# Kernel tuning notes

Hardware: AMD Instinct MI355X
Metric: run time of the kernel (lower is better)

Reference implementation:

```python
import jax, jax.numpy as jnp
import numpy as np

NEG_SLOPE = 0.01  # torch F.leaky_relu default

def setup_inputs() -> dict:
    key = jax.random.key(0)
    k1, k2, k3 = jax.random.split(key, 3)
    N, V, F_in, H = 32, 1024, 128, 64
    features = jax.random.normal(k1, (N, V, F_in), dtype=jnp.float32)
    # torch nn.Linear weights: W: [H, F_in], a: [1, 2H]
    W = jax.random.normal(k2, (H, F_in), dtype=jnp.float32) * (1.0 / np.sqrt(F_in))
    a = jax.random.normal(k3, (1, 2 * H), dtype=jnp.float32) * (1.0 / np.sqrt(2 * H))
    return {"features": features, "W": W, "a": a}

def reference(features, W, a):
    N, V, _ = features.shape
    H = W.shape[0]
    # h = features @ W^T : [N, V, H]
    h = jnp.einsum('nvf,hf->nvh', features, W)
    # The concat-linear trick decomposes: a([h_i ; h_j]) = h_i @ a_src + h_j @ a_dst
    a_src = a[0, :H]   # [H]
    a_dst = a[0, H:]   # [H]
    s_src = h @ a_src  # [N, V]  (score contribution of node i)
    s_dst = h @ a_dst  # [N, V]  (score contribution of node j)
    e = s_src[:, :, None] + s_dst[:, None, :]          # [N, V, V]
    e = jnp.where(e >= 0, e, NEG_SLOPE * e)            # leaky_relu
    attention = jax.nn.softmax(e, axis=2)              # softmax over j
    h_prime = jnp.einsum('nij,njh->nih', attention, h) # [N, V, H]
    return h_prime
```

## Files before the change

kernel.cpp:

```cpp
#include <hip/hip_runtime.h>
#include <hip/hip_bf16.h>

#define NEG_SLOPE 0.01f

constexpr int N_G  = 32;
constexpr int V_N  = 1024;
constexpr int F_IN = 128;
constexpr int H_D  = 64;
constexpr int NV   = N_G * V_N;

typedef __attribute__((ext_vector_type(8))) short bf16x8;
typedef __attribute__((ext_vector_type(4))) float f32x4;


__global__ __launch_bounds__(256) void gat_h_kernel(
    const float* __restrict__ feat,
    const float* __restrict__ W,
    const float* __restrict__ a,
    __hip_bfloat16* __restrict__ hT,
    float* __restrict__ s_src,
    float* __restrict__ s_dst)
{
    __shared__ float Fs[64][65];
    __shared__ float WsT[64][64];
    __shared__ float red[2][4][64];

    const int tid = threadIdx.x;
    const int row = tid & 63;
    const int hq  = tid >> 6;
    const int r0  = blockIdx.x * 64;

    float acc[16];
#pragma unroll
    for (int c = 0; c < 16; ++c) acc[c] = 0.f;

    for (int kh = 0; kh < 2; ++kh) {
        __syncthreads();
#pragma unroll
        for (int t = 0; t < 4; ++t) {
            int f4 = tid + t * 256;
            int rr = f4 >> 4;
            int kk = (f4 & 15) << 2;
            float4 v = *reinterpret_cast<const float4*>(
                feat + (size_t)(r0 + rr) * F_IN + kh * 64 + kk);
            Fs[rr][kk + 0] = v.x; Fs[rr][kk + 1] = v.y;
            Fs[rr][kk + 2] = v.z; Fs[rr][kk + 3] = v.w;
        }
#pragma unroll
        for (int t = 0; t < 4; ++t) {
            int f4 = tid + t * 256;
            int hh = f4 >> 4;
            int kk = (f4 & 15) << 2;
            float4 v = *reinterpret_cast<const float4*>(
                W + (size_t)hh * F_IN + kh * 64 + kk);
            WsT[kk + 0][hh] = v.x; WsT[kk + 1][hh] = v.y;
            WsT[kk + 2][hh] = v.z; WsT[kk + 3][hh] = v.w;
        }
        __syncthreads();
#pragma unroll 8
        for (int k = 0; k < 64; ++k) {
            float fv = Fs[row][k];
            const float4* wrow = reinterpret_cast<const float4*>(&WsT[k][hq * 16]);
            float wv[16];
            *reinterpret_cast<float4*>(&wv[0])  = wrow[0];
            *reinterpret_cast<float4*>(&wv[4])  = wrow[1];
            *reinterpret_cast<float4*>(&wv[8])  = wrow[2];
            *reinterpret_cast<float4*>(&wv[12]) = wrow[3];
#pragma unroll
            for (int c = 0; c < 16; ++c) acc[c] += fv * wv[c];
        }
    }

    float ps = 0.f, pd = 0.f;
#pragma unroll
    for (int c = 0; c < 16; ++c) {
        ps += acc[c] * a[hq * 16 + c];
        pd += acc[c] * a[H_D + hq * 16 + c];
    }
    red[0][hq][row] = ps;
    red[1][hq][row] = pd;

    {
        const int g   = r0 >> 10;
        const int rl  = (r0 & (V_N - 1)) + row;
        const int jt  = rl >> 6;
        const int j   = rl & 63;
        const int kk  = (j >> 5) & 1;
        const int kg  = (j >> 3) & 3;
        const int r   = j & 7;
        char* tile = (char*)(hT + (size_t)g * H_D * V_N) + (size_t)jt * 8192;
#pragma unroll
        for (int cc = 0; cc < 16; ++cc) {
            int byteoff = ((((hq * 2 + kk) * 64) + kg * 16 + cc) << 4) + (r << 1);
            *reinterpret_cast<__hip_bfloat16*>(tile + byteoff) = __float2bfloat16(acc[cc]);
        }
    }

    __syncthreads();
    if (tid < 64) {
        s_src[r0 + tid] = red[0][0][tid] + red[0][1][tid] + red[0][2][tid] + red[0][3][tid];
    } else if (tid < 128) {
        int r = tid - 64;
        s_dst[r0 + r] = red[1][0][r] + red[1][1][r] + red[1][2][r] + red[1][3][r];
    }
}

__global__ __launch_bounds__(256) void gat_attn_mfma(
    const __hip_bfloat16* __restrict__ hT,
    const float* __restrict__ s_src,
    const float* __restrict__ s_dst,
    float* __restrict__ out)
{
    __shared__ float sd[V_N];
    __shared__ float wred[4];
    __shared__ int4 hbuf[2][512];

    const int tid  = threadIdx.x;
    const int lane = tid & 63;
    const int wv   = tid >> 6;
    const int m    = lane & 15;
    const int kg   = lane >> 4;
    const int n    = blockIdx.x >> 4;
    const int i0   = (blockIdx.x & 15) * 64;
    const size_t nbase = (size_t)n * V_N;

    const char* hTg = (const char*)(hT + (size_t)n * H_D * V_N);

    float lm;
    {
        float4 v = *reinterpret_cast<const float4*>(s_dst + nbase + tid * 4);
        *reinterpret_cast<float4*>(&sd[tid * 4]) = v;
        lm = fmaxf(fmaxf(v.x, v.y), fmaxf(v.z, v.w));
    }
#pragma unroll
    for (int off = 32; off >= 1; off >>= 1)
        lm = fmaxf(lm, __shfl_xor(lm, off));
    if (lane == 0) wred[wv] = lm;

    const int row  = i0 + wv * 16 + m;
    const float ss = s_src[nbase + row];

    {
        int4 s0 = *reinterpret_cast<const int4*>(hTg + tid * 32);
        int4 s1 = *reinterpret_cast<const int4*>(hTg + tid * 32 + 16);
        hbuf[0][tid * 2]     = s0;
        hbuf[0][tid * 2 + 1] = s1;
    }
    __syncthreads();

    const float M    = fmaxf(fmaxf(wred[0], wred[1]), fmaxf(wred[2], wred[3]));
    const float t0   = ss + M;
    const float negm = -fmaxf(t0, NEG_SLOPE * t0);

    f32x4 accC[4];
    f32x4 accD = {0.f, 0.f, 0.f, 0.f};
#pragma unroll
    for (int t = 0; t < 4; ++t) accC[t] = (f32x4){0.f, 0.f, 0.f, 0.f};

    bf16x8 ones;
#pragma unroll
    for (int r = 0; r < 8; ++r) ones[r] = (short)0x3F80;

    int cur = 0;
    for (int jt = 0; jt < V_N / 64; ++jt) {
        int4 n0, n1;
        if (jt < V_N / 64 - 1) {
            const char* g = hTg + (size_t)(jt + 1) * 8192 + tid * 32;
            n0 = *reinterpret_cast<const int4*>(g);
            n1 = *reinterpret_cast<const int4*>(g + 16);
        }

        const char* bb = (const char*)&hbuf[cur][0];
#pragma unroll
        for (int kk = 0; kk < 2; ++kk) {
            float p[8];
            *reinterpret_cast<float4*>(&p[0]) =
                *reinterpret_cast<const float4*>(&sd[jt * 64 + kk * 32 + kg * 8]);
            *reinterpret_cast<float4*>(&p[4]) =
                *reinterpret_cast<const float4*>(&sd[jt * 64 + kk * 32 + kg * 8 + 4]);

            bf16x8 A;
#pragma unroll
            for (int r = 0; r < 8; ++r) {
                float tt = ss + p[r];
                float l  = fmaxf(tt, NEG_SLOPE * tt);
                float w  = __expf(l + negm);
                A[r] = (short)__builtin_bit_cast(unsigned short, __float2bfloat16(w));
            }

            accD = __builtin_amdgcn_mfma_f32_16x16x32_bf16(A, ones, accD, 0, 0, 0);
#pragma unroll
            for (int t = 0; t < 4; ++t) {
                bf16x8 B = *reinterpret_cast<const bf16x8*>(
                    bb + (t * 2 + kk) * 1024 + lane * 16);
                accC[t] = __builtin_amdgcn_mfma_f32_16x16x32_bf16(A, B, accC[t], 0, 0, 0);
            }
        }

        if (jt < V_N / 64 - 1) {
            hbuf[cur ^ 1][tid * 2]     = n0;
            hbuf[cur ^ 1][tid * 2 + 1] = n1;
        }
        __syncthreads();
        cur ^= 1;
    }

    float inv[4];
#pragma unroll
    for (int r = 0; r < 4; ++r) inv[r] = 1.0f / accD[r];
#pragma unroll
    for (int r = 0; r < 4; ++r) {
        const size_t ob = (nbase + i0 + wv * 16 + kg * 4 + r) * H_D;
#pragma unroll
        for (int t = 0; t < 4; ++t)
            out[ob + t * 16 + m] = accC[t][r] * inv[r];
    }
}

extern "C" void kernel_launch(void* const* d_in, const int* in_sizes, int n_in,
                              void* d_out, int out_size, void* d_ws, size_t ws_size,
                              hipStream_t stream) {
    const float* feat = (const float*)d_in[0];
    const float* W    = (const float*)d_in[1];
    const float* a    = (const float*)d_in[2];
    float* out = (float*)d_out;

    __hip_bfloat16* hT = (__hip_bfloat16*)d_ws;
    float* s_src = (float*)(hT + (size_t)NV * H_D);
    float* s_dst = s_src + NV;

    gat_h_kernel<<<NV / 64, 256, 0, stream>>>(feat, W, a, hT, s_src, s_dst);
    gat_attn_mfma<<<N_G * (V_N / 64), 256, 0, stream>>>(hT, s_src, s_dst, out);
}
```

Baseline: 96.86 us.

## Compute node projection with split-bf16 MFMA instead of scalar FP32 FMAs

Replaces the scalar FP32 FMA projection kernel with one that uses bf16 MFMA instructions. Both features and W are split into high and low bf16 parts, and three MFMAs per tile approximate FP32 accuracy. The output is transposed through LDS so each thread writes the packed hT tile as one 16-byte store, replacing scattered 2-byte stores. It adds conversion overhead and a larger LDS footprint, and only the first of the two kernels changes.

New measurement: 89.74 us. 1.08x faster.

```diff
diff --git a/kernel.cpp b/kernel.cpp
--- a/kernel.cpp
+++ b/kernel.cpp
@@ -12,8 +12,16 @@
 typedef __attribute__((ext_vector_type(8))) short bf16x8;
 typedef __attribute__((ext_vector_type(4))) float f32x4;
 
-
-__global__ __launch_bounds__(256) void gat_h_kernel(
+__device__ __forceinline__ float bf16bits_to_f32(unsigned short u) {
+    unsigned int x = ((unsigned int)u) << 16;
+    return __builtin_bit_cast(float, x);
+}
+__device__ __forceinline__ unsigned short f32_to_bf16bits(float f) {
+    return __builtin_bit_cast(unsigned short, __float2bfloat16(f));
+}
+
+
+__global__ __launch_bounds__(256) void gat_h_mfma(
     const float* __restrict__ feat,
     const float* __restrict__ W,
     const float* __restrict__ a,
@@ -21,87 +29,140 @@
     float* __restrict__ s_src,
     float* __restrict__ s_dst)
 {
-    __shared__ float Fs[64][65];
-    __shared__ float WsT[64][64];
-    __shared__ float red[2][4][64];
-
-    const int tid = threadIdx.x;
-    const int row = tid & 63;
-    const int hq  = tid >> 6;
-    const int r0  = blockIdx.x * 64;
-
-    float acc[16];
-#pragma unroll
-    for (int c = 0; c < 16; ++c) acc[c] = 0.f;
-
-    for (int kh = 0; kh < 2; ++kh) {
-        __syncthreads();
+    __shared__ __align__(16) float Fs[64][132];
+    __shared__ __align__(16) unsigned short Wf[16384];
+
+    const int tid  = threadIdx.x;
+    const int lane = tid & 63;
+    const int w    = tid >> 6;
+    const int mb   = lane & 15;
+    const int kg   = lane >> 4;
+    const int r0   = blockIdx.x * 64;
+
+#pragma unroll
+    for (int t = 0; t < 8; ++t) {
+        int f4  = tid + t * 256;
+        int row = f4 >> 5;
+        int c4  = (f4 & 31) << 2;
+        float4 v = *reinterpret_cast<const float4*>(
+            feat + (size_t)(r0 + row) * F_IN + c4);
+        *reinterpret_cast<float4*>(&Fs[row][c4]) = v;
+    }
+#pragma unroll
+    for (int t = 0; t < 8; ++t) {
+        int f4 = tid + t * 256;
+        int n  = f4 >> 5;
+        int k4 = (f4 & 31) << 2;
+        float4 v = *reinterpret_cast<const float4*>(W + (size_t)n * F_IN + k4);
+        int ks  = k4 >> 5;
+        int kgw = (k4 >> 3) & 3;
+        int rr  = k4 & 7;
+        int tt  = n >> 4, nn = n & 15;
+        float fv[4] = {v.x, v.y, v.z, v.w};
+        unsigned long long ph = 0, pl = 0;
+#pragma unroll
+        for (int e = 0; e < 4; ++e) {
+            unsigned short hb = f32_to_bf16bits(fv[e]);
+            unsigned short lb = f32_to_bf16bits(fv[e] - bf16bits_to_f32(hb));
+            ph |= ((unsigned long long)hb) << (16 * e);
+            pl |= ((unsigned long long)lb) << (16 * e);
+        }
+        char* base = (char*)Wf;
+        int chunk  = (ks * 4 + tt) * 2;
+        int off    = (kgw * 16 + nn) * 16 + rr * 2;
+        *reinterpret_cast<unsigned long long*>(base + chunk * 1024 + off)       = ph;
+        *reinterpret_cast<unsigned long long*>(base + (chunk + 1) * 1024 + off) = pl;
+    }
+    __syncthreads();
+
+    f32x4 acc[4];
+#pragma unroll
+    for (int t = 0; t < 4; ++t) acc[t] = (f32x4){0.f, 0.f, 0.f, 0.f};
+
+    const char* wfb = (const char*)Wf;
+#pragma unroll
+    for (int ks = 0; ks < 4; ++ks) {
+        float af[8];
+        *reinterpret_cast<float4*>(&af[0]) =
+            *reinterpret_cast<const float4*>(&Fs[w * 16 + mb][ks * 32 + kg * 8]);
+        *reinterpret_cast<float4*>(&af[4]) =
+            *reinterpret_cast<const float4*>(&Fs[w * 16 + mb][ks * 32 + kg * 8 + 4]);
+        bf16x8 Ah, Al;
+#pragma unroll
+        for (int e = 0; e < 8; ++e) {
+            unsigned short hb = f32_to_bf16bits(af[e]);
+            Ah[e] = (short)hb;
+            Al[e] = (short)f32_to_bf16bits(af[e] - bf16bits_to_f32(hb));
+        }
 #pragma unroll
         for (int t = 0; t < 4; ++t) {
-            int f4 = tid + t * 256;
-            int rr = f4 >> 4;
-            int kk = (f4 & 15) << 2;
-            float4 v = *reinterpret_cast<const float4*>(
-                feat + (size_t)(r0 + rr) * F_IN + kh * 64 + kk);
-            Fs[rr][kk + 0] = v.x; Fs[rr][kk + 1] = v.y;
-            Fs[rr][kk + 2] = v.z; Fs[rr][kk + 3] = v.w;
-        }
-#pragma unroll
-        for (int t = 0; t < 4; ++t) {
-            int f4 = tid + t * 256;
-            int hh = f4 >> 4;
-            int kk = (f4 & 15) << 2;
-            float4 v = *reinterpret_cast<const float4*>(
-                W + (size_t)hh * F_IN + kh * 64 + kk);
-            WsT[kk + 0][hh] = v.x; WsT[kk + 1][hh] = v.y;
-            WsT[kk + 2][hh] = v.z; WsT[kk + 3][hh] = v.w;
-        }
-        __syncthreads();
-#pragma unroll 8
-        for (int k = 0; k < 64; ++k) {
-            float fv = Fs[row][k];
-            const float4* wrow = reinterpret_cast<const float4*>(&WsT[k][hq * 16]);
-            float wv[16];
-            *reinterpret_cast<float4*>(&wv[0])  = wrow[0];
-            *reinterpret_cast<float4*>(&wv[4])  = wrow[1];
-            *reinterpret_cast<float4*>(&wv[8])  = wrow[2];
-            *reinterpret_cast<float4*>(&wv[12]) = wrow[3];
-#pragma unroll
-            for (int c = 0; c < 16; ++c) acc[c] += fv * wv[c];
-        }
-    }
-
-    float ps = 0.f, pd = 0.f;
-#pragma unroll
-    for (int c = 0; c < 16; ++c) {
-        ps += acc[c] * a[hq * 16 + c];
-        pd += acc[c] * a[H_D + hq * 16 + c];
-    }
-    red[0][hq][row] = ps;
-    red[1][hq][row] = pd;
-
-    {
-        const int g   = r0 >> 10;
-        const int rl  = (r0 & (V_N - 1)) + row;
-        const int jt  = rl >> 6;
-        const int j   = rl & 63;
-        const int kk  = (j >> 5) & 1;
-        const int kg  = (j >> 3) & 3;
-        const int r   = j & 7;
-        char* tile = (char*)(hT + (size_t)g * H_D * V_N) + (size_t)jt * 8192;
-#pragma unroll
-        for (int cc = 0; cc < 16; ++cc) {
-            int byteoff = ((((hq * 2 + kk) * 64) + kg * 16 + cc) << 4) + (r << 1);
-            *reinterpret_cast<__hip_bfloat16*>(tile + byteoff) = __float2bfloat16(acc[cc]);
-        }
-    }
-
-    __syncthreads();
-    if (tid < 64) {
-        s_src[r0 + tid] = red[0][0][tid] + red[0][1][tid] + red[0][2][tid] + red[0][3][tid];
-    } else if (tid < 128) {
-        int r = tid - 64;
-        s_dst[r0 + r] = red[1][0][r] + red[1][1][r] + red[1][2][r] + red[1][3][r];
+            bf16x8 Bh = *reinterpret_cast<const bf16x8*>(
+                wfb + (size_t)((ks * 4 + t) * 2) * 1024 + lane * 16);
+            bf16x8 Bl = *reinterpret_cast<const bf16x8*>(
+                wfb + (size_t)((ks * 4 + t) * 2 + 1) * 1024 + lane * 16);
+            acc[t] = __builtin_amdgcn_mfma_f32_16x16x32_bf16(Al, Bh, acc[t], 0, 0, 0);
+            acc[t] = __builtin_amdgcn_mfma_f32_16x16x32_bf16(Ah, Bl, acc[t], 0, 0, 0);
+            acc[t] = __builtin_amdgcn_mfma_f32_16x16x32_bf16(Ah, Bh, acc[t], 0, 0, 0);
+        }
+    }
+
+    float asrc[4], adst[4];
+#pragma unroll
+    for (int t = 0; t < 4; ++t) {
+        asrc[t] = a[t * 16 + mb];
+        adst[t] = a[H_D + t * 16 + mb];
+    }
+    float ps[4], pd[4];
+#pragma unroll
+    for (int reg = 0; reg < 4; ++reg) {
+        ps[reg] = acc[0][reg] * asrc[0] + acc[1][reg] * asrc[1]
+                + acc[2][reg] * asrc[2] + acc[3][reg] * asrc[3];
+        pd[reg] = acc[0][reg] * adst[0] + acc[1][reg] * adst[1]
+                + acc[2][reg] * adst[2] + acc[3][reg] * adst[3];
+    }
+#pragma unroll
+    for (int off = 1; off < 16; off <<= 1) {
+#pragma unroll
+        for (int reg = 0; reg < 4; ++reg) {
+            ps[reg] += __shfl_xor(ps[reg], off);
+            pd[reg] += __shfl_xor(pd[reg], off);
+        }
+    }
+    if (mb == 0) {
+#pragma unroll
+        for (int reg = 0; reg < 4; ++reg) {
+            int j = w * 16 + kg * 4 + reg;
+            s_src[r0 + j] = ps[reg];
+            s_dst[r0 + j] = pd[reg];
+        }
+    }
+
+    __syncthreads();
+    float (*FsT)[65] = reinterpret_cast<float(*)[65]>(&Fs[0][0]);
+#pragma unroll
+    for (int t = 0; t < 4; ++t)
+#pragma unroll
+        for (int reg = 0; reg < 4; ++reg)
+            FsT[w * 16 + kg * 4 + reg][t * 16 + mb] = acc[t][reg];
+    __syncthreads();
+
+    const int g  = r0 >> 10;
+    const int jt = (r0 & (V_N - 1)) >> 6;
+    char* tile = (char*)(hT + (size_t)g * H_D * V_N) + (size_t)jt * 8192;
+#pragma unroll
+    for (int ch = 0; ch < 2; ++ch) {
+        int chi = tid * 2 + ch;
+        int tp  = chi >> 7;
+        int kk  = (chi >> 6) & 1;
+        int kgp = (chi >> 4) & 3;
+        int mp  = chi & 15;
+        int c   = tp * 16 + mp;
+        int jb  = kk * 32 + kgp * 8;
+        unsigned short outp[8];
+#pragma unroll
+        for (int rr = 0; rr < 8; ++rr) outp[rr] = f32_to_bf16bits(FsT[jb + rr][c]);
+        *reinterpret_cast<int4*>(tile + (size_t)chi * 16) =
+            *reinterpret_cast<const int4*>(outp);
     }
 }
 
@@ -229,6 +290,6 @@
     float* s_src = (float*)(hT + (size_t)NV * H_D);
     float* s_dst = s_src + NV;
 
-    gat_h_kernel<<<NV / 64, 256, 0, stream>>>(feat, W, a, hT, s_src, s_dst);
+    gat_h_mfma<<<NV / 64, 256, 0, stream>>>(feat, W, a, hT, s_src, s_dst);
     gat_attn_mfma<<<N_G * (V_N / 64), 256, 0, stream>>>(hT, s_src, s_dst, out);
 }
```
